# Kernel optimization log

Measured on AMD Instinct MI355X. Metric: run time of the kernel, lower is better.

Reference implementation:

```python
import jax, jax.numpy as jnp
import numpy as np

B, S, D, H = 1, 4096, 1024, 16
DH = D // H

def setup_inputs() -> dict:
    key = jax.random.key(0)
    ks = jax.random.split(key, 5)
    std = float(np.sqrt(2.0 / (D + D)))
    return {
        "x": jax.random.normal(ks[0], (B, S, D), dtype=jnp.float32),
        "Wq": jax.random.normal(ks[1], (D, D), dtype=jnp.float32) * std,
        "Wk": jax.random.normal(ks[2], (D, D), dtype=jnp.float32) * std,
        "Wv": jax.random.normal(ks[3], (D, D), dtype=jnp.float32) * std,
        "Wo": jax.random.normal(ks[4], (D, D), dtype=jnp.float32) * std,
    }

def reference(x, Wq, Wk, Wv, Wo):
    # projections: input @ W.T, then split heads: b s (h d) -> b h s d
    def split_heads(t):
        b, s, _ = t.shape
        return t.reshape(b, s, H, DH).transpose(0, 2, 1, 3)
    q = split_heads(x @ Wq.T)
    k = split_heads(x @ Wk.T)
    v = split_heads(x @ Wv.T)
    scale = 1.0 / jnp.sqrt(jnp.asarray(DH, dtype=x.dtype))
    scores = jnp.einsum("bhqd,bhkd->bhqk", q, k) * scale  # (b,h,s,s)
    # causal mask: allow k <= q
    causal = jnp.tril(jnp.ones((S, S), dtype=bool))
    scores = jnp.where(causal, scores, jnp.finfo(scores.dtype).min)
    attn = jax.nn.softmax(scores, axis=-1)
    out = jnp.einsum("bhqk,bhkd->bhqd", attn, v)  # (b,h,s,d)
    out = out.transpose(0, 2, 1, 3).reshape(B, S, D)  # b h s d -> b s (h d)
    return out @ Wo.T
```

## Files before the change

kernel.cpp:

```cpp
#include <hip/hip_runtime.h>
#include <math.h>

#define SEQ 4096
#define DM  1024
#define NH  16
#define DH  64
#define NS  4

typedef _Float16 h16;
typedef __attribute__((ext_vector_type(4))) _Float16 h16x4;
typedef __attribute__((ext_vector_type(8))) _Float16 h16x8;
typedef __attribute__((ext_vector_type(4))) float f32x4;

__device__ __forceinline__ void gload_lds16(const h16* g, h16* l) {
    __builtin_amdgcn_global_load_lds(
        (const __attribute__((address_space(1))) void*)g,
        (__attribute__((address_space(3))) void*)l, 16, 0, 0);
}

__global__ __launch_bounds__(256) void cvt_all(const float* __restrict__ x,
                                               const float* __restrict__ wq,
                                               const float* __restrict__ wk,
                                               const float* __restrict__ wv,
                                               const float* __restrict__ wo,
                                               h16* __restrict__ dst) {
    const size_t SD4 = (size_t)SEQ * DM / 4;
    const size_t DD4 = (size_t)DM * DM / 4;
    const size_t i = (size_t)blockIdx.x * 256 + threadIdx.x;
    const float* src;
    size_t off;
    if (i < SD4) { src = x; off = i; }
    else {
        const size_t j = i - SD4;
        const int wsel = (int)(j >> 18);
        off = j & (DD4 - 1);
        src = (wsel == 0) ? wq : (wsel == 1) ? wk : (wsel == 2) ? wv : wo;
    }
    const float4 v = ((const float4*)src)[off];
    h16x4 o = { (h16)v.x, (h16)v.y, (h16)v.z, (h16)v.w };
    ((h16x4*)dst)[i] = o;
}

#define GT 32

__global__ __launch_bounds__(256) void gemm_qkv(const h16* __restrict__ xh,
                                                const h16* __restrict__ Wq,
                                                const h16* __restrict__ Wk,
                                                const h16* __restrict__ Wv,
                                                h16* __restrict__ Qh,
                                                h16* __restrict__ Kh,
                                                h16* __restrict__ Vth,
                                                float scl) {
    __shared__ h16 As[2][128 * GT];
    __shared__ h16 Bs[2][128 * GT];

    const int z    = blockIdx.z;
    const h16* B   = (z == 0) ? Wq : (z == 1) ? Wk : Wv;
    const int t    = threadIdx.x;
    const int lane = t & 63;
    const int w    = t >> 6;
    const int wm   = (w >> 1) * 64;
    const int wn   = (w & 1) * 64;
    const int l15  = lane & 15;
    const int lq   = lane >> 4;
    const int lq8  = lq * 8;
    const int m0   = blockIdx.y * 128;
    const int n0   = blockIdx.x * 128;
    const int K = DM, M = SEQ, N = DM;

    const int srow = w * 16 + (lane >> 2);
    const int scol = (lane & 3) * 8;
    const h16* pa0 = xh + (size_t)(m0 + srow) * K + scol;
    const h16* pa1 = xh + (size_t)(m0 + 64 + srow) * K + scol;
    const h16* pb0 = B  + (size_t)(n0 + srow) * K + scol;
    const h16* pb1 = B  + (size_t)(n0 + 64 + srow) * K + scol;

    f32x4 acc[4][4] = {};

    for (int k0 = 0; k0 < K; k0 += 64) {
        __syncthreads();
        #pragma unroll
        for (int s = 0; s < 2; ++s) {
            const int ko = k0 + s * 32;
            gload_lds16(pa0 + ko, &As[s][w * 512]);
            gload_lds16(pa1 + ko, &As[s][2048 + w * 512]);
            gload_lds16(pb0 + ko, &Bs[s][w * 512]);
            gload_lds16(pb1 + ko, &Bs[s][2048 + w * 512]);
        }
        __syncthreads();

        #pragma unroll
        for (int s = 0; s < 2; ++s) {
            h16x8 af[4], bf[4];
            #pragma unroll
            for (int i = 0; i < 4; ++i)
                af[i] = *(const h16x8*)&As[s][(wm + i * 16 + l15) * GT + lq8];
            #pragma unroll
            for (int j = 0; j < 4; ++j)
                bf[j] = *(const h16x8*)&Bs[s][(wn + j * 16 + l15) * GT + lq8];
            #pragma unroll
            for (int i = 0; i < 4; ++i)
                #pragma unroll
                for (int j = 0; j < 4; ++j)
                    acc[i][j] = __builtin_amdgcn_mfma_f32_16x16x32_f16(af[i], bf[j], acc[i][j], 0, 0, 0);
        }
    }

    const int cr = wm + lq * 4;
    const int cc = wn + l15;
    if (z == 2) {
        #pragma unroll
        for (int i = 0; i < 4; ++i)
            #pragma unroll
            for (int j = 0; j < 4; ++j) {
                const int gm0 = m0 + cr + i * 16;
                const int gn  = n0 + cc + j * 16;
                h16x4 v = { (h16)acc[i][j][0], (h16)acc[i][j][1],
                            (h16)acc[i][j][2], (h16)acc[i][j][3] };
                *(h16x4*)(Vth + (size_t)gn * M + gm0) = v;
            }
    } else {
        h16* Og = (z == 0) ? Qh : Kh;
        const float e = (z == 0) ? scl : 1.0f;
        #pragma unroll
        for (int i = 0; i < 4; ++i)
            #pragma unroll
            for (int j = 0; j < 4; ++j)
                #pragma unroll
                for (int r = 0; r < 4; ++r) {
                    const int gm = m0 + cr + i * 16 + r;
                    const int gn = n0 + cc + j * 16;
                    Og[(size_t)gm * N + gn] = (h16)(acc[i][j][r] * e);
                }
    }
}

__global__ __launch_bounds__(256) void gemm_out(const h16* __restrict__ A,
                                                const h16* __restrict__ B,
                                                float* __restrict__ C) {
    __shared__ h16 As[2][64 * GT];
    __shared__ h16 Bs[2][128 * GT];

    const int t    = threadIdx.x;
    const int lane = t & 63;
    const int w    = t >> 6;
    const int wm   = (w >> 1) * 32;
    const int wn   = (w & 1) * 64;
    const int l15  = lane & 15;
    const int lq   = lane >> 4;
    const int lq8  = lq * 8;
    const int m0   = blockIdx.y * 64;
    const int n0   = blockIdx.x * 128;
    const int K = DM, N = DM;

    const int srow = w * 16 + (lane >> 2);
    const int scol = (lane & 3) * 8;
    const h16* pa0 = A + (size_t)(m0 + srow) * K + scol;
    const h16* pb0 = B + (size_t)(n0 + srow) * K + scol;
    const h16* pb1 = B + (size_t)(n0 + 64 + srow) * K + scol;

    f32x4 acc[2][4] = {};

    for (int k0 = 0; k0 < K; k0 += 64) {
        __syncthreads();
        #pragma unroll
        for (int s = 0; s < 2; ++s) {
            const int ko = k0 + s * 32;
            gload_lds16(pa0 + ko, &As[s][w * 512]);
            gload_lds16(pb0 + ko, &Bs[s][w * 512]);
            gload_lds16(pb1 + ko, &Bs[s][2048 + w * 512]);
        }
        __syncthreads();

        #pragma unroll
        for (int s = 0; s < 2; ++s) {
            h16x8 af[2], bf[4];
            #pragma unroll
            for (int i = 0; i < 2; ++i)
                af[i] = *(const h16x8*)&As[s][(wm + i * 16 + l15) * GT + lq8];
            #pragma unroll
            for (int j = 0; j < 4; ++j)
                bf[j] = *(const h16x8*)&Bs[s][(wn + j * 16 + l15) * GT + lq8];
            #pragma unroll
            for (int i = 0; i < 2; ++i)
                #pragma unroll
                for (int j = 0; j < 4; ++j)
                    acc[i][j] = __builtin_amdgcn_mfma_f32_16x16x32_f16(af[i], bf[j], acc[i][j], 0, 0, 0);
        }
    }

    const int cr = wm + lq * 4;
    const int cc = wn + l15;
    #pragma unroll
    for (int i = 0; i < 2; ++i)
        #pragma unroll
        for (int j = 0; j < 4; ++j)
            #pragma unroll
            for (int r = 0; r < 4; ++r)
                C[(size_t)(m0 + cr + i * 16 + r) * N + n0 + cc + j * 16] = acc[i][j][r];
}

#define AST 80
#define VST 72

__global__ __launch_bounds__(256, 3) void flash_attn_split(
        const h16* __restrict__ Qg, const h16* __restrict__ Kg,
        const h16* __restrict__ Vt, h16* __restrict__ OP,
        float* __restrict__ Mb, float* __restrict__ Lb) {
    __shared__ h16 Ks[2][64 * AST];
    __shared__ h16 Vs[2][64 * VST];

    const int jq   = 31 - (int)blockIdx.y;
    const int hh   = blockIdx.x;
    const int sp   = blockIdx.z;
    const int t    = threadIdx.x;
    const int lane = t & 63;
    const int w    = t >> 6;
    const int l15  = lane & 15;
    const int lq   = lane >> 4;
    const int lq8  = lq * 8;
    const int hc   = hh * DH;
    const int q0   = jq * 128;
    const int qa   = w * 16 + l15;
    const int diag1 = 2 * jq;
    const int diag2 = 2 * jq + 1;

    const int ntile = 2 * jq + 2;
    const int chunk = (ntile + NS - 1) / NS;
    const int kts   = sp * chunk;
    const int kte   = (kts + chunk < ntile) ? (kts + chunk) : ntile;

    const int r1 = t >> 3;
    const int r2 = r1 + 32;
    const int c1 = (t & 7) * 8;

    const size_t qrow1 = (size_t)(q0 + qa) * DM + hc;
    const size_t qrow2 = (size_t)(q0 + 64 + qa) * DM + hc;
    h16x8 qf[2][2];
    qf[0][0] = *(const h16x8*)(Qg + qrow1 + lq8);
    qf[0][1] = *(const h16x8*)(Qg + qrow1 + 32 + lq8);
    qf[1][0] = *(const h16x8*)(Qg + qrow2 + lq8);
    qf[1][1] = *(const h16x8*)(Qg + qrow2 + 32 + lq8);

    const int kb0 = kts * 64;
    h16x8 kv1 = *(const h16x8*)(Kg + (size_t)(kb0 + r1) * DM + hc + c1);
    h16x8 kv2 = *(const h16x8*)(Kg + (size_t)(kb0 + r2) * DM + hc + c1);
    h16x8 vv1 = *(const h16x8*)(Vt + (size_t)(hc + r1) * SEQ + kb0 + c1);
    h16x8 vv2 = *(const h16x8*)(Vt + (size_t)(hc + r2) * SEQ + kb0 + c1);

    float m_st[2] = { -1e30f, -1e30f };
    float l_st[2] = { 0.0f, 0.0f };
    f32x4 o[2][4] = {};
    int bb = 0;

    for (int kt = kts; kt < kte; ++kt) {
        *(h16x8*)&Ks[bb][r1 * AST + c1] = kv1;
        *(h16x8*)&Ks[bb][r2 * AST + c1] = kv2;
        *(h16x8*)&Vs[bb][r1 * VST + c1] = vv1;
        *(h16x8*)&Vs[bb][r2 * VST + c1] = vv2;
        __syncthreads();
        if (kt + 1 < kte) {
            const int k0n = (kt + 1) * 64;
            kv1 = *(const h16x8*)(Kg + (size_t)(k0n + r1) * DM + hc + c1);
            kv2 = *(const h16x8*)(Kg + (size_t)(k0n + r2) * DM + hc + c1);
            vv1 = *(const h16x8*)(Vt + (size_t)(hc + r1) * SEQ + k0n + c1);
            vv2 = *(const h16x8*)(Vt + (size_t)(hc + r2) * SEQ + k0n + c1);
        }

        f32x4 s[2][4] = {};
        #pragma unroll
        for (int kc = 0; kc < 2; ++kc) {
            h16x8 kf[4];
            #pragma unroll
            for (int jj = 0; jj < 4; ++jj)
                kf[jj] = *(const h16x8*)&Ks[bb][(jj * 16 + l15) * AST + kc * 32 + lq8];
            #pragma unroll
            for (int jj = 0; jj < 4; ++jj)
                s[0][jj] = __builtin_amdgcn_mfma_f32_16x16x32_f16(kf[jj], qf[0][kc], s[0][jj], 0, 0, 0);
            #pragma unroll
            for (int jj = 0; jj < 4; ++jj)
                s[1][jj] = __builtin_amdgcn_mfma_f32_16x16x32_f16(kf[jj], qf[1][kc], s[1][jj], 0, 0, 0);
        }

        if (kt >= diag1) {
            const int rel = (q0 + qa) - kt * 64;
            #pragma unroll
            for (int jj = 0; jj < 4; ++jj)
                #pragma unroll
                for (int r = 0; r < 4; ++r)
                    if ((jj * 16 + lq * 4 + r) > rel) s[0][jj][r] = -1e30f;
        }
        if (kt >= diag2) {
            const int rel = (q0 + 64 + qa) - kt * 64;
            #pragma unroll
            for (int jj = 0; jj < 4; ++jj)
                #pragma unroll
                for (int r = 0; r < 4; ++r)
                    if ((jj * 16 + lq * 4 + r) > rel) s[1][jj][r] = -1e30f;
        }

        h16x4 pk[2][4];
        #pragma unroll
        for (int h = 0; h < 2; ++h) {
            float mx = -1e30f;
            #pragma unroll
            for (int jj = 0; jj < 4; ++jj)
                #pragma unroll
                for (int r = 0; r < 4; ++r)
                    mx = fmaxf(mx, s[h][jj][r]);
            mx = fmaxf(mx, __shfl_xor(mx, 16, 64));
            mx = fmaxf(mx, __shfl_xor(mx, 32, 64));
            if (mx > m_st[h] + 5.0f) {
                const float alpha = exp2f(m_st[h] - mx);
                m_st[h] = mx;
                l_st[h] *= alpha;
                #pragma unroll
                for (int jj = 0; jj < 4; ++jj)
                    #pragma unroll
                    for (int r = 0; r < 4; ++r)
                        o[h][jj][r] *= alpha;
            }
            #pragma unroll
            for (int jj = 0; jj < 4; ++jj) {
                const float p0 = exp2f(s[h][jj][0] - m_st[h]);
                const float p1 = exp2f(s[h][jj][1] - m_st[h]);
                const float p2 = exp2f(s[h][jj][2] - m_st[h]);
                const float p3 = exp2f(s[h][jj][3] - m_st[h]);
                l_st[h] += (p0 + p1) + (p2 + p3);
                pk[h][jj] = h16x4{ (h16)p0, (h16)p1, (h16)p2, (h16)p3 };
            }
        }

        #pragma unroll
        for (int dd = 0; dd < 4; ++dd)
            #pragma unroll
            for (int jj = 0; jj < 4; ++jj) {
                const h16x4 vf = *(const h16x4*)&Vs[bb][(dd * 16 + l15) * VST + jj * 16 + lq * 4];
                o[0][dd] = __builtin_amdgcn_mfma_f32_16x16x16f16(vf, pk[0][jj], o[0][dd], 0, 0, 0);
                o[1][dd] = __builtin_amdgcn_mfma_f32_16x16x16f16(vf, pk[1][jj], o[1][dd], 0, 0, 0);
            }

        bb ^= 1;
    }

    #pragma unroll
    for (int h = 0; h < 2; ++h) {
        l_st[h] += __shfl_xor(l_st[h], 16, 64);
        l_st[h] += __shfl_xor(l_st[h], 32, 64);
    }

    h16* const op = OP + (size_t)sp * SEQ * DM;
    #pragma unroll
    for (int h = 0; h < 2; ++h) {
        const int qg_row = q0 + h * 64 + qa;
        const size_t qg = (size_t)qg_row * DM + hc;
        #pragma unroll
        for (int jj = 0; jj < 4; ++jj) {
            h16x4 ov = { (h16)o[h][jj][0], (h16)o[h][jj][1],
                         (h16)o[h][jj][2], (h16)o[h][jj][3] };
            *(h16x4*)(op + qg + jj * 16 + lq * 4) = ov;
        }
        if (lq == 0) {
            const size_t mi = ((size_t)sp * NH + hh) * SEQ + qg_row;
            Mb[mi] = m_st[h];
            Lb[mi] = l_st[h];
        }
    }
}

__global__ __launch_bounds__(256) void combine(const h16* __restrict__ OP,
                                               const float* __restrict__ Mb,
                                               const float* __restrict__ Lb,
                                               h16* __restrict__ AOh) {
    const int i  = blockIdx.x * 256 + threadIdx.x;
    const int q  = i >> 8;
    const int c4 = (i & 255) * 4;
    const int hh = c4 >> 6;

    float ms[NS], ls[NS];
    float mstar = -1e30f;
    #pragma unroll
    for (int s = 0; s < NS; ++s) {
        const size_t mi = ((size_t)s * NH + hh) * SEQ + q;
        ms[s] = Mb[mi];
        ls[s] = Lb[mi];
        mstar = fmaxf(mstar, ms[s]);
    }
    float L = 0.0f;
    float acc[4] = {};
    #pragma unroll
    for (int s = 0; s < NS; ++s) {
        const float ws = exp2f(ms[s] - mstar);
        L += ls[s] * ws;
        const h16x4 ov = *(const h16x4*)(OP + (size_t)s * SEQ * DM + (size_t)q * DM + c4);
        acc[0] += ws * (float)ov[0];
        acc[1] += ws * (float)ov[1];
        acc[2] += ws * (float)ov[2];
        acc[3] += ws * (float)ov[3];
    }
    const float inv = 1.0f / L;
    h16x4 r = { (h16)(acc[0] * inv), (h16)(acc[1] * inv),
                (h16)(acc[2] * inv), (h16)(acc[3] * inv) };
    *(h16x4*)(AOh + (size_t)q * DM + c4) = r;
}

extern "C" void kernel_launch(void* const* d_in, const int* in_sizes, int n_in,
                              void* d_out, int out_size, void* d_ws, size_t ws_size,
                              hipStream_t stream) {
    const float* x  = (const float*)d_in[0];
    const float* Wq = (const float*)d_in[1];
    const float* Wk = (const float*)d_in[2];
    const float* Wv = (const float*)d_in[3];
    const float* Wo = (const float*)d_in[4];
    float* out = (float*)d_out;

    const size_t SD = (size_t)SEQ * DM;
    const size_t DD = (size_t)DM * DM;

    h16* xh  = (h16*)d_ws;
    h16* wqh = xh + SD;
    h16* wkh = wqh + DD;
    h16* wvh = wkh + DD;
    h16* woh = wvh + DD;
    h16* Qh  = woh + DD;
    h16* Kh  = Qh + SD;
    h16* Vth = Kh + SD;
    h16* AOh = Vth + SD;
    h16* OP  = AOh + SD;
    float* Mb = (float*)(OP + (size_t)NS * SD);
    float* Lb = Mb + (size_t)NS * NH * SEQ;

    const dim3 blk(256);

    cvt_all<<<(int)((SD + 4 * DD) / 4 / 256), blk, 0, stream>>>(x, Wq, Wk, Wv, Wo, xh);

    const float SCL = 0.125f * 1.44269504088896340736f;

    gemm_qkv<<<dim3(DM / 128, SEQ / 128, 3), blk, 0, stream>>>(
        xh, wqh, wkh, wvh, Qh, Kh, Vth, SCL);

    flash_attn_split<<<dim3(NH, 32, NS), blk, 0, stream>>>(Qh, Kh, Vth, OP, Mb, Lb);

    combine<<<(int)(SD / 4 / 256), blk, 0, stream>>>(OP, Mb, Lb, AOh);

    gemm_out<<<dim3(DM / 128, SEQ / 64), blk, 0, stream>>>(AOh, woh, out);
}
```

Measured before the change: 221.4 us.

## Load K/V fragments directly from global into registers, dropping LDS staging

Removes the shared-memory double buffer and barriers in the split flash-attention kernel. Each wave now loads its K and V MFMA fragments straight from global memory, with K for the next tile prefetched into registers using ping-pong buffers and a manually unrolled two-step loop. It also skips the cross-lane max shuffle when no lane exceeds the running max threshold, and lowers the occupancy hint to two blocks per SM. In exchange, each of the four waves re-reads the same K/V tiles from global/L2 with smaller, less coalesced accesses, and register pressure goes up.

```diff
diff --git a/kernel.cpp b/kernel.cpp
--- a/kernel.cpp
+++ b/kernel.cpp
@@ -200,16 +200,102 @@
                 C[(size_t)(m0 + cr + i * 16 + r) * N + n0 + cc + j * 16] = acc[i][j][r];
 }
 
-#define AST 80
-#define VST 72
-
-__global__ __launch_bounds__(256, 3) void flash_attn_split(
+__device__ __forceinline__ void attn_step(
+        int kt, bool pref,
+        const h16* __restrict__ Kg, const h16* __restrict__ Vt,
+        int l15, int lq, int lq8, int hc, int q0, int qa,
+        int diag1, int diag2,
+        h16x8 (&cur)[2][4], h16x8 (&nxt)[2][4],
+        h16x8 (&qf)[2][2],
+        float (&m_st)[2], float (&l_st)[2], f32x4 (&o)[2][4]) {
+    h16x4 vf[4][4];
+    #pragma unroll
+    for (int dd = 0; dd < 4; ++dd)
+        #pragma unroll
+        for (int jj = 0; jj < 4; ++jj)
+            vf[dd][jj] = *(const h16x4*)(Vt + (size_t)(hc + dd * 16 + l15) * SEQ
+                                         + kt * 64 + jj * 16 + lq * 4);
+    if (pref) {
+        #pragma unroll
+        for (int kc = 0; kc < 2; ++kc)
+            #pragma unroll
+            for (int jj = 0; jj < 4; ++jj)
+                nxt[kc][jj] = *(const h16x8*)(Kg + (size_t)((kt + 1) * 64 + jj * 16 + l15) * DM
+                                              + hc + kc * 32 + lq8);
+    }
+
+    f32x4 s[2][4] = {};
+    #pragma unroll
+    for (int kc = 0; kc < 2; ++kc)
+        #pragma unroll
+        for (int jj = 0; jj < 4; ++jj) {
+            s[0][jj] = __builtin_amdgcn_mfma_f32_16x16x32_f16(cur[kc][jj], qf[0][kc], s[0][jj], 0, 0, 0);
+            s[1][jj] = __builtin_amdgcn_mfma_f32_16x16x32_f16(cur[kc][jj], qf[1][kc], s[1][jj], 0, 0, 0);
+        }
+
+    if (kt >= diag1) {
+        const int rel = (q0 + qa) - kt * 64;
+        #pragma unroll
+        for (int jj = 0; jj < 4; ++jj)
+            #pragma unroll
+            for (int r = 0; r < 4; ++r)
+                if ((jj * 16 + lq * 4 + r) > rel) s[0][jj][r] = -1e30f;
+    }
+    if (kt >= diag2) {
+        const int rel = (q0 + 64 + qa) - kt * 64;
+        #pragma unroll
+        for (int jj = 0; jj < 4; ++jj)
+            #pragma unroll
+            for (int r = 0; r < 4; ++r)
+                if ((jj * 16 + lq * 4 + r) > rel) s[1][jj][r] = -1e30f;
+    }
+
+    h16x4 pk[2][4];
+    #pragma unroll
+    for (int h = 0; h < 2; ++h) {
+        const float a0 = fmaxf(fmaxf(s[h][0][0], s[h][0][1]), fmaxf(s[h][0][2], s[h][0][3]));
+        const float a1 = fmaxf(fmaxf(s[h][1][0], s[h][1][1]), fmaxf(s[h][1][2], s[h][1][3]));
+        const float a2 = fmaxf(fmaxf(s[h][2][0], s[h][2][1]), fmaxf(s[h][2][2], s[h][2][3]));
+        const float a3 = fmaxf(fmaxf(s[h][3][0], s[h][3][1]), fmaxf(s[h][3][2], s[h][3][3]));
+        const float mxl = fmaxf(fmaxf(a0, a1), fmaxf(a2, a3));
+        if (!__all(mxl <= m_st[h] + 5.0f)) {
+            float mx = fmaxf(mxl, __shfl_xor(mxl, 16, 64));
+            mx = fmaxf(mx, __shfl_xor(mx, 32, 64));
+            if (mx > m_st[h] + 5.0f) {
+                const float alpha = exp2f(m_st[h] - mx);
+                m_st[h] = mx;
+                l_st[h] *= alpha;
+                #pragma unroll
+                for (int jj = 0; jj < 4; ++jj)
+                    #pragma unroll
+                    for (int r = 0; r < 4; ++r)
+                        o[h][jj][r] *= alpha;
+            }
+        }
+        #pragma unroll
+        for (int jj = 0; jj < 4; ++jj) {
+            const float p0 = exp2f(s[h][jj][0] - m_st[h]);
+            const float p1 = exp2f(s[h][jj][1] - m_st[h]);
+            const float p2 = exp2f(s[h][jj][2] - m_st[h]);
+            const float p3 = exp2f(s[h][jj][3] - m_st[h]);
+            l_st[h] += (p0 + p1) + (p2 + p3);
+            pk[h][jj] = h16x4{ (h16)p0, (h16)p1, (h16)p2, (h16)p3 };
+        }
+    }
+
+    #pragma unroll
+    for (int dd = 0; dd < 4; ++dd)
+        #pragma unroll
+        for (int jj = 0; jj < 4; ++jj) {
+            o[0][dd] = __builtin_amdgcn_mfma_f32_16x16x16f16(vf[dd][jj], pk[0][jj], o[0][dd], 0, 0, 0);
+            o[1][dd] = __builtin_amdgcn_mfma_f32_16x16x16f16(vf[dd][jj], pk[1][jj], o[1][dd], 0, 0, 0);
+        }
+}
+
+__global__ __launch_bounds__(256, 2) void flash_attn_split(
         const h16* __restrict__ Qg, const h16* __restrict__ Kg,
         const h16* __restrict__ Vt, h16* __restrict__ OP,
         float* __restrict__ Mb, float* __restrict__ Lb) {
-    __shared__ h16 Ks[2][64 * AST];
-    __shared__ h16 Vs[2][64 * VST];
-
     const int jq   = 31 - (int)blockIdx.y;
     const int hh   = blockIdx.x;
     const int sp   = blockIdx.z;
@@ -230,10 +316,6 @@
     const int kts   = sp * chunk;
     const int kte   = (kts + chunk < ntile) ? (kts + chunk) : ntile;
 
-    const int r1 = t >> 3;
-    const int r2 = r1 + 32;
-    const int c1 = (t & 7) * 8;
-
     const size_t qrow1 = (size_t)(q0 + qa) * DM + hc;
     const size_t qrow2 = (size_t)(q0 + 64 + qa) * DM + hc;
     h16x8 qf[2][2];
@@ -242,106 +324,30 @@
     qf[1][0] = *(const h16x8*)(Qg + qrow2 + lq8);
     qf[1][1] = *(const h16x8*)(Qg + qrow2 + 32 + lq8);
 
-    const int kb0 = kts * 64;
-    h16x8 kv1 = *(const h16x8*)(Kg + (size_t)(kb0 + r1) * DM + hc + c1);
-    h16x8 kv2 = *(const h16x8*)(Kg + (size_t)(kb0 + r2) * DM + hc + c1);
-    h16x8 vv1 = *(const h16x8*)(Vt + (size_t)(hc + r1) * SEQ + kb0 + c1);
-    h16x8 vv2 = *(const h16x8*)(Vt + (size_t)(hc + r2) * SEQ + kb0 + c1);
-
     float m_st[2] = { -1e30f, -1e30f };
     float l_st[2] = { 0.0f, 0.0f };
     f32x4 o[2][4] = {};
-    int bb = 0;
-
-    for (int kt = kts; kt < kte; ++kt) {
-        *(h16x8*)&Ks[bb][r1 * AST + c1] = kv1;
-        *(h16x8*)&Ks[bb][r2 * AST + c1] = kv2;
-        *(h16x8*)&Vs[bb][r1 * VST + c1] = vv1;
-        *(h16x8*)&Vs[bb][r2 * VST + c1] = vv2;
-        __syncthreads();
-        if (kt + 1 < kte) {
-            const int k0n = (kt + 1) * 64;
-            kv1 = *(const h16x8*)(Kg + (size_t)(k0n + r1) * DM + hc + c1);
-            kv2 = *(const h16x8*)(Kg + (size_t)(k0n + r2) * DM + hc + c1);
-            vv1 = *(const h16x8*)(Vt + (size_t)(hc + r1) * SEQ + k0n + c1);
-            vv2 = *(const h16x8*)(Vt + (size_t)(hc + r2) * SEQ + k0n + c1);
-        }
-
-        f32x4 s[2][4] = {};
-        #pragma unroll
-        for (int kc = 0; kc < 2; ++kc) {
-            h16x8 kf[4];
+
+    h16x8 kfA[2][4], kfB[2][4];
+    if (kts < kte) {
+        #pragma unroll
+        for (int kc = 0; kc < 2; ++kc)
             #pragma unroll
             for (int jj = 0; jj < 4; ++jj)
-                kf[jj] = *(const h16x8*)&Ks[bb][(jj * 16 + l15) * AST + kc * 32 + lq8];
-            #pragma unroll
-            for (int jj = 0; jj < 4; ++jj)
-                s[0][jj] = __builtin_amdgcn_mfma_f32_16x16x32_f16(kf[jj], qf[0][kc], s[0][jj], 0, 0, 0);
-            #pragma unroll
-            for (int jj = 0; jj < 4; ++jj)
-                s[1][jj] = __builtin_amdgcn_mfma_f32_16x16x32_f16(kf[jj], qf[1][kc], s[1][jj], 0, 0, 0);
-        }
-
-        if (kt >= diag1) {
-            const int rel = (q0 + qa) - kt * 64;
-            #pragma unroll
-            for (int jj = 0; jj < 4; ++jj)
-                #pragma unroll
-                for (int r = 0; r < 4; ++r)
-                    if ((jj * 16 + lq * 4 + r) > rel) s[0][jj][r] = -1e30f;
-        }
-        if (kt >= diag2) {
-            const int rel = (q0 + 64 + qa) - kt * 64;
-            #pragma unroll
-            for (int jj = 0; jj < 4; ++jj)
-                #pragma unroll
-                for (int r = 0; r < 4; ++r)
-                    if ((jj * 16 + lq * 4 + r) > rel) s[1][jj][r] = -1e30f;
-        }
-
-        h16x4 pk[2][4];
-        #pragma unroll
-        for (int h = 0; h < 2; ++h) {
-            float mx = -1e30f;
-            #pragma unroll
-            for (int jj = 0; jj < 4; ++jj)
-                #pragma unroll
-                for (int r = 0; r < 4; ++r)
-                    mx = fmaxf(mx, s[h][jj][r]);
-            mx = fmaxf(mx, __shfl_xor(mx, 16, 64));
-            mx = fmaxf(mx, __shfl_xor(mx, 32, 64));
-            if (mx > m_st[h] + 5.0f) {
-                const float alpha = exp2f(m_st[h] - mx);
-                m_st[h] = mx;
-                l_st[h] *= alpha;
-                #pragma unroll
-                for (int jj = 0; jj < 4; ++jj)
-                    #pragma unroll
-                    for (int r = 0; r < 4; ++r)
-                        o[h][jj][r] *= alpha;
-            }
-            #pragma unroll
-            for (int jj = 0; jj < 4; ++jj) {
-                const float p0 = exp2f(s[h][jj][0] - m_st[h]);
-                const float p1 = exp2f(s[h][jj][1] - m_st[h]);
-                const float p2 = exp2f(s[h][jj][2] - m_st[h]);
-                const float p3 = exp2f(s[h][jj][3] - m_st[h]);
-                l_st[h] += (p0 + p1) + (p2 + p3);
-                pk[h][jj] = h16x4{ (h16)p0, (h16)p1, (h16)p2, (h16)p3 };
-            }
-        }
-
-        #pragma unroll
-        for (int dd = 0; dd < 4; ++dd)
-            #pragma unroll
-            for (int jj = 0; jj < 4; ++jj) {
-                const h16x4 vf = *(const h16x4*)&Vs[bb][(dd * 16 + l15) * VST + jj * 16 + lq * 4];
-                o[0][dd] = __builtin_amdgcn_mfma_f32_16x16x16f16(vf, pk[0][jj], o[0][dd], 0, 0, 0);
-                o[1][dd] = __builtin_amdgcn_mfma_f32_16x16x16f16(vf, pk[1][jj], o[1][dd], 0, 0, 0);
-            }
-
-        bb ^= 1;
-    }
+                kfA[kc][jj] = *(const h16x8*)(Kg + (size_t)(kts * 64 + jj * 16 + l15) * DM
+                                              + hc + kc * 32 + lq8);
+    }
+
+    int kt = kts;
+    for (; kt + 1 < kte; kt += 2) {
+        attn_step(kt,     true,            Kg, Vt, l15, lq, lq8, hc, q0, qa,
+                  diag1, diag2, kfA, kfB, qf, m_st, l_st, o);
+        attn_step(kt + 1, (kt + 2 < kte),  Kg, Vt, l15, lq, lq8, hc, q0, qa,
+                  diag1, diag2, kfB, kfA, qf, m_st, l_st, o);
+    }
+    if (kt < kte)
+        attn_step(kt, false, Kg, Vt, l15, lq, lq8, hc, q0, qa,
+                  diag1, diag2, kfA, kfB, qf, m_st, l_st, o);
 
     #pragma unroll
     for (int h = 0; h < 2; ++h) {
```

Result: slower. 355.7 us (+60.6%).

## Single-buffer K/V LDS tiles and compute softmax row sums with MFMA

Applied to the files above, without the earlier changes.

Replaces the double-buffered K/V shared-memory tiles with a single buffer, adding an extra barrier before each store, which halves LDS use and may allow more resident blocks. The per-lane row-sum accumulation with cross-lane shuffles is replaced by MFMA ops that multiply the fp16 probabilities by a ones vector, moving the adds onto the matrix units. The sum now uses fp16-rounded probabilities. The max reduction is rewritten as a balanced tree. The extra barrier per tile serializes LDS fill with compute.

```diff
diff --git a/kernel.cpp b/kernel.cpp
--- a/kernel.cpp
+++ b/kernel.cpp
@@ -207,8 +207,8 @@
         const h16* __restrict__ Qg, const h16* __restrict__ Kg,
         const h16* __restrict__ Vt, h16* __restrict__ OP,
         float* __restrict__ Mb, float* __restrict__ Lb) {
-    __shared__ h16 Ks[2][64 * AST];
-    __shared__ h16 Vs[2][64 * VST];
+    __shared__ h16 Ks[64 * AST];
+    __shared__ h16 Vs[64 * VST];
 
     const int jq   = 31 - (int)blockIdx.y;
     const int hh   = blockIdx.x;
@@ -242,22 +242,27 @@
     qf[1][0] = *(const h16x8*)(Qg + qrow2 + lq8);
     qf[1][1] = *(const h16x8*)(Qg + qrow2 + 32 + lq8);
 
-    const int kb0 = kts * 64;
-    h16x8 kv1 = *(const h16x8*)(Kg + (size_t)(kb0 + r1) * DM + hc + c1);
-    h16x8 kv2 = *(const h16x8*)(Kg + (size_t)(kb0 + r2) * DM + hc + c1);
-    h16x8 vv1 = *(const h16x8*)(Vt + (size_t)(hc + r1) * SEQ + kb0 + c1);
-    h16x8 vv2 = *(const h16x8*)(Vt + (size_t)(hc + r2) * SEQ + kb0 + c1);
-
     float m_st[2] = { -1e30f, -1e30f };
-    float l_st[2] = { 0.0f, 0.0f };
+    f32x4 lacc[2] = {};
     f32x4 o[2][4] = {};
-    int bb = 0;
+    const h16x4 one4 = { (h16)1.0f, (h16)1.0f, (h16)1.0f, (h16)1.0f };
+
+    h16x8 kv1, kv2, vv1, vv2;
+
+    if (kts < kte) {
+        const int kb0 = kts * 64;
+        kv1 = *(const h16x8*)(Kg + (size_t)(kb0 + r1) * DM + hc + c1);
+        kv2 = *(const h16x8*)(Kg + (size_t)(kb0 + r2) * DM + hc + c1);
+        vv1 = *(const h16x8*)(Vt + (size_t)(hc + r1) * SEQ + kb0 + c1);
+        vv2 = *(const h16x8*)(Vt + (size_t)(hc + r2) * SEQ + kb0 + c1);
+    }
 
     for (int kt = kts; kt < kte; ++kt) {
-        *(h16x8*)&Ks[bb][r1 * AST + c1] = kv1;
-        *(h16x8*)&Ks[bb][r2 * AST + c1] = kv2;
-        *(h16x8*)&Vs[bb][r1 * VST + c1] = vv1;
-        *(h16x8*)&Vs[bb][r2 * VST + c1] = vv2;
+        __syncthreads();
+        *(h16x8*)&Ks[r1 * AST + c1] = kv1;
+        *(h16x8*)&Ks[r2 * AST + c1] = kv2;
+        *(h16x8*)&Vs[r1 * VST + c1] = vv1;
+        *(h16x8*)&Vs[r2 * VST + c1] = vv2;
         __syncthreads();
         if (kt + 1 < kte) {
             const int k0n = (kt + 1) * 64;
@@ -273,7 +278,7 @@
             h16x8 kf[4];
             #pragma unroll
             for (int jj = 0; jj < 4; ++jj)
-                kf[jj] = *(const h16x8*)&Ks[bb][(jj * 16 + l15) * AST + kc * 32 + lq8];
+                kf[jj] = *(const h16x8*)&Ks[(jj * 16 + l15) * AST + kc * 32 + lq8];
             #pragma unroll
             for (int jj = 0; jj < 4; ++jj)
                 s[0][jj] = __builtin_amdgcn_mfma_f32_16x16x32_f16(kf[jj], qf[0][kc], s[0][jj], 0, 0, 0);
@@ -302,18 +307,18 @@
         h16x4 pk[2][4];
         #pragma unroll
         for (int h = 0; h < 2; ++h) {
-            float mx = -1e30f;
-            #pragma unroll
-            for (int jj = 0; jj < 4; ++jj)
-                #pragma unroll
-                for (int r = 0; r < 4; ++r)
-                    mx = fmaxf(mx, s[h][jj][r]);
+            const float a0 = fmaxf(fmaxf(s[h][0][0], s[h][0][1]), fmaxf(s[h][0][2], s[h][0][3]));
+            const float a1 = fmaxf(fmaxf(s[h][1][0], s[h][1][1]), fmaxf(s[h][1][2], s[h][1][3]));
+            const float a2 = fmaxf(fmaxf(s[h][2][0], s[h][2][1]), fmaxf(s[h][2][2], s[h][2][3]));
+            const float a3 = fmaxf(fmaxf(s[h][3][0], s[h][3][1]), fmaxf(s[h][3][2], s[h][3][3]));
+            float mx = fmaxf(fmaxf(a0, a1), fmaxf(a2, a3));
             mx = fmaxf(mx, __shfl_xor(mx, 16, 64));
             mx = fmaxf(mx, __shfl_xor(mx, 32, 64));
             if (mx > m_st[h] + 5.0f) {
                 const float alpha = exp2f(m_st[h] - mx);
                 m_st[h] = mx;
-                l_st[h] *= alpha;
+                #pragma unroll
+                for (int r = 0; r < 4; ++r) lacc[h][r] *= alpha;
                 #pragma unroll
                 for (int jj = 0; jj < 4; ++jj)
                     #pragma unroll
@@ -326,27 +331,21 @@
                 const float p1 = exp2f(s[h][jj][1] - m_st[h]);
                 const float p2 = exp2f(s[h][jj][2] - m_st[h]);
                 const float p3 = exp2f(s[h][jj][3] - m_st[h]);
-                l_st[h] += (p0 + p1) + (p2 + p3);
                 pk[h][jj] = h16x4{ (h16)p0, (h16)p1, (h16)p2, (h16)p3 };
             }
+            #pragma unroll
+            for (int jj = 0; jj < 4; ++jj)
+                lacc[h] = __builtin_amdgcn_mfma_f32_16x16x16f16(one4, pk[h][jj], lacc[h], 0, 0, 0);
         }
 
         #pragma unroll
         for (int dd = 0; dd < 4; ++dd)
             #pragma unroll
             for (int jj = 0; jj < 4; ++jj) {
-                const h16x4 vf = *(const h16x4*)&Vs[bb][(dd * 16 + l15) * VST + jj * 16 + lq * 4];
+                const h16x4 vf = *(const h16x4*)&Vs[(dd * 16 + l15) * VST + jj * 16 + lq * 4];
                 o[0][dd] = __builtin_amdgcn_mfma_f32_16x16x16f16(vf, pk[0][jj], o[0][dd], 0, 0, 0);
                 o[1][dd] = __builtin_amdgcn_mfma_f32_16x16x16f16(vf, pk[1][jj], o[1][dd], 0, 0, 0);
             }
-
-        bb ^= 1;
-    }
-
-    #pragma unroll
-    for (int h = 0; h < 2; ++h) {
-        l_st[h] += __shfl_xor(l_st[h], 16, 64);
-        l_st[h] += __shfl_xor(l_st[h], 32, 64);
     }
 
     h16* const op = OP + (size_t)sp * SEQ * DM;
@@ -363,7 +362,7 @@
         if (lq == 0) {
             const size_t mi = ((size_t)sp * NH + hh) * SEQ + qg_row;
             Mb[mi] = m_st[h];
-            Lb[mi] = l_st[h];
+            Lb[mi] = lacc[h][0];
         }
     }
 }
```

Result: no change. 222.1 us (+0.3%).
